# Kernel optimization log

Measured on AMD Instinct MI355X. Metric: run time of the kernel, lower is better.

## Reference

```python
import jax, jax.numpy as jnp
import numpy as np

EPS = 1e-9


def _squash(s, axis=-1):
    # squash(s) = (|s|^2 / (1+|s|^2)) * s / |s|
    sq = jnp.sum(jnp.square(s), axis=axis, keepdims=True)
    norm = jnp.sqrt(sq + EPS)
    return (sq / (1.0 + sq)) * (s / norm)


def setup_inputs() -> dict:
    key = jax.random.key(0)
    B, N_IN, N_OUT, ATOMS = 32, 2048, 64, 16
    votes = jax.random.normal(key, (B, N_IN, N_OUT, ATOMS), dtype=jnp.float32)
    return {"votes": votes, "num_routing": 3}


def reference(votes, num_routing):
    # votes: [B, in_caps, out_caps, atoms]
    temper = 1.0
    softmax_in = False
    B, n_in, n_out, atoms = votes.shape
    logits = jnp.zeros((B, n_in, n_out, 1), dtype=votes.dtype)
    pose = None
    for i in range(num_routing):
        # coupling coefficients: softmax over out-caps axis (softmax_in=False)
        ax = 1 if softmax_in else 2
        c = jax.nn.softmax(logits * temper, axis=ax)  # [B, in, out, 1]
        # weighted pooling over input capsules -> [B, 1, out, atoms]
        preact = jnp.sum(c * votes, axis=1, keepdims=True)
        pose = _squash(preact, axis=-1)
        if i < num_routing - 1:
            # agreement: <votes, pose> over atoms -> [B, in, out, 1]
            logits = logits + jnp.sum(votes * pose, axis=-1, keepdims=True)
    prob = jnp.sqrt(jnp.sum(jnp.square(pose), axis=-1, keepdims=True) + EPS)  # [B,1,out,1]
    pose_out = jnp.squeeze(pose, axis=-3)          # [B, out, atoms]
    prob_out = jnp.squeeze(prob, axis=(-3, -1))    # [B, out]
    return pose_out, prob_out
```

## Files before the change

kernel.cpp:

```cpp
#include <hip/hip_runtime.h>


#define NB 32
#define NIN 2048
#define NOUT 64
#define ATOMS 16
#define EPSF 1e-9f

#define ROWS_PER_WAVE 8
#define WAVES_PER_BLOCK 4
#define ROWS_PER_BLOCK (ROWS_PER_WAVE * WAVES_PER_BLOCK)
#define CHUNKS (NIN / ROWS_PER_BLOCK)
#define RBATCH 2

template <int USE_POSE>
__global__ __launch_bounds__(256, 4) void route_pass(
    const float4* __restrict__ votes4,
    const float4* __restrict__ pose_accum4,
    float4* __restrict__ partials4)
{
    const int b     = blockIdx.x / CHUNKS;
    const int chunk = blockIdx.x % CHUNKS;
    const int wave  = threadIdx.x >> 6;
    const int lane  = threadIdx.x & 63;

    float4 pse[4];
    if (USE_POSE) {
#pragma unroll
        for (int j = 0; j < 4; ++j)
            pse[j] = pose_accum4[(b * NOUT + j * 16 + (lane >> 2)) * 4 + (lane & 3)];
    }

    float4 acc[4];
#pragma unroll
    for (int j = 0; j < 4; ++j) acc[j] = make_float4(0.f, 0.f, 0.f, 0.f);

    const int in0 = chunk * ROWS_PER_BLOCK + wave * ROWS_PER_WAVE;
    const float4* vrow = votes4 + (size_t)(b * NIN + in0) * 256 + lane;

    for (int r0 = 0; r0 < ROWS_PER_WAVE; r0 += RBATCH) {
        float4 v[RBATCH][4];
#pragma unroll
        for (int r = 0; r < RBATCH; ++r) {
            const float4* vp = vrow + (size_t)(r0 + r) * 256;
#pragma unroll
            for (int j = 0; j < 4; ++j) v[r][j] = vp[j * 64];
        }

        if (USE_POSE) {
            float lg[RBATCH][4];
#pragma unroll
            for (int r = 0; r < RBATCH; ++r)
#pragma unroll
                for (int j = 0; j < 4; ++j) {
                    float d = v[r][j].x * pse[j].x;
                    d = fmaf(v[r][j].y, pse[j].y, d);
                    d = fmaf(v[r][j].z, pse[j].z, d);
                    d = fmaf(v[r][j].w, pse[j].w, d);
                    lg[r][j] = d;
                }
#pragma unroll
            for (int mask = 1; mask <= 2; mask <<= 1)
#pragma unroll
                for (int r = 0; r < RBATCH; ++r)
#pragma unroll
                    for (int j = 0; j < 4; ++j)
                        lg[r][j] += __shfl_xor(lg[r][j], mask, 64);

            float e[RBATCH][4], s[RBATCH];
#pragma unroll
            for (int r = 0; r < RBATCH; ++r) {
                float t = 0.f;
#pragma unroll
                for (int j = 0; j < 4; ++j) { e[r][j] = __expf(lg[r][j]); t += e[r][j]; }
                s[r] = t;
            }
#pragma unroll
            for (int mask = 4; mask <= 32; mask <<= 1)
#pragma unroll
                for (int r = 0; r < RBATCH; ++r)
                    s[r] += __shfl_xor(s[r], mask, 64);

#pragma unroll
            for (int r = 0; r < RBATCH; ++r) {
                float inv = __frcp_rn(s[r]);
#pragma unroll
                for (int j = 0; j < 4; ++j) {
                    float c = e[r][j] * inv;
                    acc[j].x = fmaf(c, v[r][j].x, acc[j].x);
                    acc[j].y = fmaf(c, v[r][j].y, acc[j].y);
                    acc[j].z = fmaf(c, v[r][j].z, acc[j].z);
                    acc[j].w = fmaf(c, v[r][j].w, acc[j].w);
                }
            }
        } else {
#pragma unroll
            for (int r = 0; r < RBATCH; ++r)
#pragma unroll
                for (int j = 0; j < 4; ++j) {
                    acc[j].x += v[r][j].x; acc[j].y += v[r][j].y;
                    acc[j].z += v[r][j].z; acc[j].w += v[r][j].w;
                }
        }
    }
    if (!USE_POSE) {
#pragma unroll
        for (int j = 0; j < 4; ++j) {
            acc[j].x *= (1.f / 64.f); acc[j].y *= (1.f / 64.f);
            acc[j].z *= (1.f / 64.f); acc[j].w *= (1.f / 64.f);
        }
    }

    __shared__ float4 red4[WAVES_PER_BLOCK * 256];
#pragma unroll
    for (int j = 0; j < 4; ++j)
        red4[wave * 256 + j * 64 + lane] = acc[j];
    __syncthreads();

    float4* pblock4 = partials4 + ((size_t)(b * CHUNKS + chunk) << 8);
    {
        int idx = threadIdx.x;
        float4 a = red4[idx], b2 = red4[256 + idx], c = red4[512 + idx], d = red4[768 + idx];
        float4 t;
        t.x = (a.x + b2.x) + (c.x + d.x);
        t.y = (a.y + b2.y) + (c.y + d.y);
        t.z = (a.z + b2.z) + (c.z + d.z);
        t.w = (a.w + b2.w) + (c.w + d.w);
        pblock4[idx] = t;
    }
}

__global__ __launch_bounds__(256) void squash_reduce(
    const float* __restrict__ partials,
    float* __restrict__ pose_accum,
    float* __restrict__ d_out,
    int mode)
{
    int gid = blockIdx.x * 256 + threadIdx.x;
    int b  = gid >> 10;
    int oa = gid & 1023;
    const float* p = partials + ((size_t)b << 16) + oa;
    float s0 = 0.f, s1 = 0.f, s2 = 0.f, s3 = 0.f;
#pragma unroll
    for (int c = 0; c < CHUNKS; c += 4) {
        s0 += p[(c + 0) << 10];
        s1 += p[(c + 1) << 10];
        s2 += p[(c + 2) << 10];
        s3 += p[(c + 3) << 10];
    }
    float s = (s0 + s1) + (s2 + s3);

    float sq = s * s;
#pragma unroll
    for (int mask = 1; mask < ATOMS; mask <<= 1)
        sq += __shfl_xor(sq, mask, 64);
    float norm = sqrtf(sq + EPSF);
    float f = (sq / (1.0f + sq)) / norm;
    float pse = f * s;
    if (mode == 0) {
        pose_accum[gid] = pse;
    } else if (mode == 1) {
        pose_accum[gid] += pse;
    } else {
        d_out[gid] = pse;
        if ((gid & (ATOMS - 1)) == 0) {
            float psq = f * f * sq;
            d_out[NB * NOUT * ATOMS + (gid >> 4)] = sqrtf(psq + EPSF);
        }
    }
}

extern "C" void kernel_launch(void* const* d_in, const int* in_sizes, int n_in,
                              void* d_out, int out_size, void* d_ws, size_t ws_size,
                              hipStream_t stream) {
    const float4* votes4 = (const float4*)d_in[0];
    float* out = (float*)d_out;

    float* pose_accum = (float*)d_ws;
    float* partials   = pose_accum + NB * NOUT * ATOMS;

    dim3 blk(256);
    dim3 grid_route(NB * CHUNKS);
    dim3 grid_sq(NB * NOUT * ATOMS / 256);

    route_pass<0><<<grid_route, blk, 0, stream>>>(votes4, nullptr, (float4*)partials);
    squash_reduce<<<grid_sq, blk, 0, stream>>>(partials, pose_accum, nullptr, 0);

    route_pass<1><<<grid_route, blk, 0, stream>>>(votes4, (const float4*)pose_accum, (float4*)partials);
    squash_reduce<<<grid_sq, blk, 0, stream>>>(partials, pose_accum, nullptr, 1);

    route_pass<1><<<grid_route, blk, 0, stream>>>(votes4, (const float4*)pose_accum, (float4*)partials);
    squash_reduce<<<grid_sq, blk, 0, stream>>>(partials, nullptr, out, 2);
}
```

Measured before the change: 446.4 us.

## Cache fp16 copy of votes in first pass and read it in later routing passes

The first routing pass now writes a half-precision copy of the votes into workspace while summing them. The two later passes read that copy instead of the fp32 votes, with the lane mapping reworked so each lane handles eight atoms per load. This halves the bytes read by the later passes of a bandwidth-bound kernel, but adds a large write in pass 0, lowers vote precision to fp16, and needs a much larger workspace.

```diff
diff --git a/kernel.cpp b/kernel.cpp
--- a/kernel.cpp
+++ b/kernel.cpp
@@ -1,4 +1,5 @@
 #include <hip/hip_runtime.h>
+#include <hip/hip_fp16.h>
 
 
 #define NB 32
@@ -13,9 +14,88 @@
 #define CHUNKS (NIN / ROWS_PER_BLOCK)
 #define RBATCH 2
 
-template <int USE_POSE>
-__global__ __launch_bounds__(256, 4) void route_pass(
+__device__ __forceinline__ uint2 pack_h2(const float4& v) {
+    __half2 a = __floats2half2_rn(v.x, v.y);
+    __half2 b = __floats2half2_rn(v.z, v.w);
+    uint2 r;
+    r.x = *reinterpret_cast<const unsigned*>(&a);
+    r.y = *reinterpret_cast<const unsigned*>(&b);
+    return r;
+}
+
+__device__ __forceinline__ void unpack8(const uint4& u, float* v) {
+    const __half2* h = reinterpret_cast<const __half2*>(&u);
+#pragma unroll
+    for (int k = 0; k < 4; ++k) {
+        float2 f = __half22float2(h[k]);
+        v[2 * k] = f.x; v[2 * k + 1] = f.y;
+    }
+}
+
+__global__ __launch_bounds__(256, 4) void route_pass0(
     const float4* __restrict__ votes4,
+    uint2* __restrict__ votes_h2,
+    float4* __restrict__ partials4)
+{
+    const int b     = blockIdx.x / CHUNKS;
+    const int chunk = blockIdx.x % CHUNKS;
+    const int wave  = threadIdx.x >> 6;
+    const int lane  = threadIdx.x & 63;
+
+    float4 acc[4];
+#pragma unroll
+    for (int j = 0; j < 4; ++j) acc[j] = make_float4(0.f, 0.f, 0.f, 0.f);
+
+    const int in0 = chunk * ROWS_PER_BLOCK + wave * ROWS_PER_WAVE;
+    const float4* vrow = votes4   + (size_t)(b * NIN + in0) * 256 + lane;
+    uint2*        hrow = votes_h2 + (size_t)(b * NIN + in0) * 256 + lane;
+
+    for (int r0 = 0; r0 < ROWS_PER_WAVE; r0 += RBATCH) {
+        float4 v[RBATCH][4];
+#pragma unroll
+        for (int r = 0; r < RBATCH; ++r) {
+            const float4* vp = vrow + (size_t)(r0 + r) * 256;
+#pragma unroll
+            for (int j = 0; j < 4; ++j) v[r][j] = vp[j * 64];
+        }
+#pragma unroll
+        for (int r = 0; r < RBATCH; ++r) {
+            uint2* hp = hrow + (size_t)(r0 + r) * 256;
+#pragma unroll
+            for (int j = 0; j < 4; ++j) {
+                hp[j * 64] = pack_h2(v[r][j]);
+                acc[j].x += v[r][j].x; acc[j].y += v[r][j].y;
+                acc[j].z += v[r][j].z; acc[j].w += v[r][j].w;
+            }
+        }
+    }
+#pragma unroll
+    for (int j = 0; j < 4; ++j) {
+        acc[j].x *= (1.f / 64.f); acc[j].y *= (1.f / 64.f);
+        acc[j].z *= (1.f / 64.f); acc[j].w *= (1.f / 64.f);
+    }
+
+    __shared__ float4 red4[WAVES_PER_BLOCK * 256];
+#pragma unroll
+    for (int j = 0; j < 4; ++j)
+        red4[wave * 256 + j * 64 + lane] = acc[j];
+    __syncthreads();
+
+    float4* pblock4 = partials4 + ((size_t)(b * CHUNKS + chunk) << 8);
+    {
+        int idx = threadIdx.x;
+        float4 a = red4[idx], b2 = red4[256 + idx], c = red4[512 + idx], d = red4[768 + idx];
+        float4 t;
+        t.x = (a.x + b2.x) + (c.x + d.x);
+        t.y = (a.y + b2.y) + (c.y + d.y);
+        t.z = (a.z + b2.z) + (c.z + d.z);
+        t.w = (a.w + b2.w) + (c.w + d.w);
+        pblock4[idx] = t;
+    }
+}
+
+__global__ __launch_bounds__(256, 4) void route_passN(
+    const uint4* __restrict__ votes_h4,
     const float4* __restrict__ pose_accum4,
     float4* __restrict__ partials4)
 {
@@ -23,98 +103,88 @@
     const int chunk = blockIdx.x % CHUNKS;
     const int wave  = threadIdx.x >> 6;
     const int lane  = threadIdx.x & 63;
-
-    float4 pse[4];
-    if (USE_POSE) {
-#pragma unroll
-        for (int j = 0; j < 4; ++j)
-            pse[j] = pose_accum4[(b * NOUT + j * 16 + (lane >> 2)) * 4 + (lane & 3)];
-    }
-
-    float4 acc[4];
-#pragma unroll
-    for (int j = 0; j < 4; ++j) acc[j] = make_float4(0.f, 0.f, 0.f, 0.f);
+    const int h     = lane & 1;
+    const int oq    = lane >> 1;
+
+    float pose[2][8];
+#pragma unroll
+    for (int j = 0; j < 2; ++j) {
+        int base = (b * NOUT + j * 32 + oq) * 4 + 2 * h;
+        float4 a = pose_accum4[base];
+        float4 c = pose_accum4[base + 1];
+        pose[j][0] = a.x; pose[j][1] = a.y; pose[j][2] = a.z; pose[j][3] = a.w;
+        pose[j][4] = c.x; pose[j][5] = c.y; pose[j][6] = c.z; pose[j][7] = c.w;
+    }
+
+    float acc[2][8];
+#pragma unroll
+    for (int j = 0; j < 2; ++j)
+#pragma unroll
+        for (int k = 0; k < 8; ++k) acc[j][k] = 0.f;
 
     const int in0 = chunk * ROWS_PER_BLOCK + wave * ROWS_PER_WAVE;
-    const float4* vrow = votes4 + (size_t)(b * NIN + in0) * 256 + lane;
+    const uint4* vrow = votes_h4 + (size_t)(b * NIN + in0) * 128 + lane;
 
     for (int r0 = 0; r0 < ROWS_PER_WAVE; r0 += RBATCH) {
-        float4 v[RBATCH][4];
-#pragma unroll
-        for (int r = 0; r < RBATCH; ++r) {
-            const float4* vp = vrow + (size_t)(r0 + r) * 256;
-#pragma unroll
-            for (int j = 0; j < 4; ++j) v[r][j] = vp[j * 64];
-        }
-
-        if (USE_POSE) {
-            float lg[RBATCH][4];
+        uint4 raw[RBATCH][2];
+#pragma unroll
+        for (int r = 0; r < RBATCH; ++r) {
+            const uint4* vp = vrow + (size_t)(r0 + r) * 128;
+            raw[r][0] = vp[0]; raw[r][1] = vp[64];
+        }
+        float v[RBATCH][2][8];
+        float lg[RBATCH][2];
+#pragma unroll
+        for (int r = 0; r < RBATCH; ++r)
+#pragma unroll
+            for (int j = 0; j < 2; ++j) {
+                unpack8(raw[r][j], v[r][j]);
+                float d = v[r][j][0] * pose[j][0];
+#pragma unroll
+                for (int k = 1; k < 8; ++k) d = fmaf(v[r][j][k], pose[j][k], d);
+                lg[r][j] = d;
+            }
+#pragma unroll
+        for (int r = 0; r < RBATCH; ++r)
+#pragma unroll
+            for (int j = 0; j < 2; ++j)
+                lg[r][j] += __shfl_xor(lg[r][j], 1, 64);
+
+        float e[RBATCH][2], s[RBATCH];
+#pragma unroll
+        for (int r = 0; r < RBATCH; ++r) {
+            e[r][0] = __expf(lg[r][0]);
+            e[r][1] = __expf(lg[r][1]);
+            s[r] = e[r][0] + e[r][1];
+        }
+#pragma unroll
+        for (int mask = 2; mask <= 32; mask <<= 1)
 #pragma unroll
             for (int r = 0; r < RBATCH; ++r)
-#pragma unroll
-                for (int j = 0; j < 4; ++j) {
-                    float d = v[r][j].x * pse[j].x;
-                    d = fmaf(v[r][j].y, pse[j].y, d);
-                    d = fmaf(v[r][j].z, pse[j].z, d);
-                    d = fmaf(v[r][j].w, pse[j].w, d);
-                    lg[r][j] = d;
-                }
-#pragma unroll
-            for (int mask = 1; mask <= 2; mask <<= 1)
-#pragma unroll
-                for (int r = 0; r < RBATCH; ++r)
-#pragma unroll
-                    for (int j = 0; j < 4; ++j)
-                        lg[r][j] += __shfl_xor(lg[r][j], mask, 64);
-
-            float e[RBATCH][4], s[RBATCH];
-#pragma unroll
-            for (int r = 0; r < RBATCH; ++r) {
-                float t = 0.f;
-#pragma unroll
-                for (int j = 0; j < 4; ++j) { e[r][j] = __expf(lg[r][j]); t += e[r][j]; }
-                s[r] = t;
+                s[r] += __shfl_xor(s[r], mask, 64);
+
+#pragma unroll
+        for (int r = 0; r < RBATCH; ++r) {
+            float inv = __frcp_rn(s[r]);
+#pragma unroll
+            for (int j = 0; j < 2; ++j) {
+                float c = e[r][j] * inv;
+#pragma unroll
+                for (int k = 0; k < 8; ++k)
+                    acc[j][k] = fmaf(c, v[r][j][k], acc[j][k]);
             }
-#pragma unroll
-            for (int mask = 4; mask <= 32; mask <<= 1)
-#pragma unroll
-                for (int r = 0; r < RBATCH; ++r)
-                    s[r] += __shfl_xor(s[r], mask, 64);
-
-#pragma unroll
-            for (int r = 0; r < RBATCH; ++r) {
-                float inv = __frcp_rn(s[r]);
-#pragma unroll
-                for (int j = 0; j < 4; ++j) {
-                    float c = e[r][j] * inv;
-                    acc[j].x = fmaf(c, v[r][j].x, acc[j].x);
-                    acc[j].y = fmaf(c, v[r][j].y, acc[j].y);
-                    acc[j].z = fmaf(c, v[r][j].z, acc[j].z);
-                    acc[j].w = fmaf(c, v[r][j].w, acc[j].w);
-                }
-            }
-        } else {
-#pragma unroll
-            for (int r = 0; r < RBATCH; ++r)
-#pragma unroll
-                for (int j = 0; j < 4; ++j) {
-                    acc[j].x += v[r][j].x; acc[j].y += v[r][j].y;
-                    acc[j].z += v[r][j].z; acc[j].w += v[r][j].w;
-                }
-        }
-    }
-    if (!USE_POSE) {
-#pragma unroll
-        for (int j = 0; j < 4; ++j) {
-            acc[j].x *= (1.f / 64.f); acc[j].y *= (1.f / 64.f);
-            acc[j].z *= (1.f / 64.f); acc[j].w *= (1.f / 64.f);
         }
     }
 
     __shared__ float4 red4[WAVES_PER_BLOCK * 256];
 #pragma unroll
-    for (int j = 0; j < 4; ++j)
-        red4[wave * 256 + j * 64 + lane] = acc[j];
+    for (int j = 0; j < 2; ++j)
+#pragma unroll
+        for (int k = 0; k < 2; ++k) {
+            float4 t = make_float4(acc[j][4 * k], acc[j][4 * k + 1],
+                                   acc[j][4 * k + 2], acc[j][4 * k + 3]);
+            red4[wave * 256 + j * 128 + oq * 4 + 2 * h + k] = t;
+        }
     __syncthreads();
 
     float4* pblock4 = partials4 + ((size_t)(b * CHUNKS + chunk) << 8);
@@ -178,17 +248,18 @@
 
     float* pose_accum = (float*)d_ws;
     float* partials   = pose_accum + NB * NOUT * ATOMS;
+    void*  votes_h    = (void*)(partials + (size_t)NB * CHUNKS * NOUT * ATOMS);
 
     dim3 blk(256);
     dim3 grid_route(NB * CHUNKS);
     dim3 grid_sq(NB * NOUT * ATOMS / 256);
 
-    route_pass<0><<<grid_route, blk, 0, stream>>>(votes4, nullptr, (float4*)partials);
+    route_pass0<<<grid_route, blk, 0, stream>>>(votes4, (uint2*)votes_h, (float4*)partials);
     squash_reduce<<<grid_sq, blk, 0, stream>>>(partials, pose_accum, nullptr, 0);
 
-    route_pass<1><<<grid_route, blk, 0, stream>>>(votes4, (const float4*)pose_accum, (float4*)partials);
+    route_passN<<<grid_route, blk, 0, stream>>>((const uint4*)votes_h, (const float4*)pose_accum, (float4*)partials);
     squash_reduce<<<grid_sq, blk, 0, stream>>>(partials, pose_accum, nullptr, 1);
 
-    route_pass<1><<<grid_route, blk, 0, stream>>>(votes4, (const float4*)pose_accum, (float4*)partials);
+    route_passN<<<grid_route, blk, 0, stream>>>((const uint4*)votes_h, (const float4*)pose_accum, (float4*)partials);
     squash_reduce<<<grid_sq, blk, 0, stream>>>(partials, nullptr, out, 2);
 }
```

Result: slower. 474.4 us (+6.3%).
